# Kernel tuning notes

Hardware: AMD Instinct MI355X
Metric: run time of the kernel (lower is better)

## Reference

```python
import jax, jax.numpy as jnp
import numpy as np

EPS_L2 = 1e-12  # torch F.normalize eps
EPS_NORM = 1e-5  # ZeroCenteredRMSNorm eps


def _linear(x, W, b):
    return x @ W.T + b


def _silu(x):
    return x * jax.nn.sigmoid(x)


def _l2norm(x):
    n = jnp.sqrt(jnp.sum(x * x, axis=-1, keepdims=True))
    return x / jnp.maximum(n, EPS_L2)


def _dwconv_causal(x, w, b):
    # x: [B,S,d]; w: [d,1,4] (torch depthwise conv weight); causal pad 3 left
    y = jax.lax.conv_general_dilated(
        x.transpose(0, 2, 1), w, window_strides=(1,), padding=[(3, 0)],
        dimension_numbers=('NCH', 'OIH', 'NCH'), feature_group_count=w.shape[0])
    return y.transpose(0, 2, 1) + b


def _zc_rmsnorm(x, weight):
    xm = x - jnp.mean(x, axis=-1, keepdims=True)
    var = jnp.mean(xm * xm, axis=-1, keepdims=True)
    return xm * jax.lax.rsqrt(var + EPS_NORM) * weight


def _gated_delta_core(q, k, v, alpha, beta):
    # q,k,v: [B,S,d]; alpha,beta: [B,S]
    B, S, d = q.shape
    S0 = jnp.zeros((B, d, d), dtype=q.dtype)

    def step(St, inp):
        qt, kt, vt, at, bt = inp  # [B,d],[B,d],[B,d],[B],[B]
        # S @ (a*(I - b k k^T)) = a*(S - b*(S k) k^T)   (rank-1 update, same math)
        Sk = jnp.einsum('bij,bj->bi', St, kt)            # [B,d]
        a = at[:, None, None]
        b = bt[:, None, None]
        Sn = a * (St - b * Sk[:, :, None] * kt[:, None, :]) + b * vt[:, :, None] * kt[:, None, :]
        ot = jnp.einsum('bij,bj->bi', Sn, qt)            # [B,d]
        return Sn, ot

    xs = (q.transpose(1, 0, 2), k.transpose(1, 0, 2), v.transpose(1, 0, 2),
          alpha.T, beta.T)
    _, outs = jax.lax.scan(step, S0, xs)  # outs: [S,B,d]
    return outs.transpose(1, 0, 2)


def setup_inputs() -> dict:
    key = jax.random.key(0)
    ks = jax.random.split(key, 16)
    B, S, d = 8, 2048, 512
    w = lambda k, shape: (jax.random.normal(k, shape, jnp.float32) * 0.02)
    return {
        'x': jax.random.normal(ks[0], (B, S, d), jnp.float32),
        'Wq': w(ks[1], (d, d)), 'bq': jnp.zeros((d,), jnp.float32),
        'Wk': w(ks[2], (d, d)), 'bk': jnp.zeros((d,), jnp.float32),
        'Wv': w(ks[3], (d, d)), 'bv': jnp.zeros((d,), jnp.float32),
        'Wa': w(ks[4], (1, d)), 'ba': jnp.zeros((1,), jnp.float32),
        'Wb': w(ks[5], (1, d)), 'bb': jnp.zeros((1,), jnp.float32),
        'cwq': w(ks[6], (d, 1, 4)), 'cbq': jnp.zeros((d,), jnp.float32),
        'cwk': w(ks[7], (d, 1, 4)), 'cbk': jnp.zeros((d,), jnp.float32),
        'cwv': w(ks[8], (d, 1, 4)), 'cbv': jnp.zeros((d,), jnp.float32),
        'norm_w': jnp.ones((d,), jnp.float32),
        'Wg': w(ks[9], (d, d)), 'bg': jnp.zeros((d,), jnp.float32),
        'Wo': w(ks[10], (d, d)), 'bo': jnp.zeros((d,), jnp.float32),
    }


def reference(x, Wq, bq, Wk, bk, Wv, bv, Wa, ba, Wb, bb,
              cwq, cbq, cwk, cbk, cwv, cbv, norm_w, Wg, bg, Wo, bo):
    q_c = _dwconv_causal(_linear(x, Wq, bq), cwq, cbq)
    k_c = _dwconv_causal(_linear(x, Wk, bk), cwk, cbk)
    v_c = _dwconv_causal(_linear(x, Wv, bv), cwv, cbv)
    q = _l2norm(_silu(q_c))
    k = _l2norm(_silu(k_c))
    v = _silu(v_c)
    alpha = jax.nn.sigmoid(_linear(x, Wa, ba))[..., 0]  # [B,S]
    beta = jax.nn.sigmoid(_linear(x, Wb, bb))[..., 0]   # [B,S]
    gdn = _gated_delta_core(q, k, v, alpha, beta)       # [B,S,d]
    gdn = _zc_rmsnorm(gdn, norm_w)
    gate = _silu(_linear(x, Wg, bg))
    return _linear(gdn * gate, Wo, bo)
```

## Files before the change

### kernel.cpp

```cpp
#include <hip/hip_runtime.h>
#include <math.h>

typedef unsigned short u16;
typedef unsigned int u32;
typedef short short8 __attribute__((ext_vector_type(8)));
typedef float f32x4 __attribute__((ext_vector_type(4)));

#define B_ 8
#define S_ 2048
#define D_ 512
#define N_ (B_ * S_)
#define ND_ ((size_t)N_ * D_)
#define CC_ 32
#define NC_ (S_ / CC_)
#define SV_ 16

__device__ __forceinline__ u16 f2bf(float f) {
  union { float f; u32 i; } v; v.f = f;
  u32 i = v.i;
  i += 0x7FFFu + ((i >> 16) & 1u);
  return (u16)(i >> 16);
}
__device__ __forceinline__ float bf2f(u16 u) {
  union { u32 i; float f; } v; v.i = ((u32)u) << 16; return v.f;
}
__device__ __forceinline__ float sigm(float x) { return 1.0f / (1.0f + expf(-x)); }

__global__ __launch_bounds__(256) void cvt_bf16(const float* __restrict__ s,
                                                u16* __restrict__ d, int n)
{
  const int i = (blockIdx.x * 256 + threadIdx.x) * 4;
  if (i < n) {
    const float4 v = *(const float4*)(s + i);
    ushort4 o;
    o.x = f2bf(v.x); o.y = f2bf(v.y); o.z = f2bf(v.z); o.w = f2bf(v.w);
    *(ushort4*)(d + i) = o;
  }
}

__global__ __launch_bounds__(256) void cvt_w5(
    const float* __restrict__ w0, const float* __restrict__ w1,
    const float* __restrict__ w2, const float* __restrict__ w3,
    const float* __restrict__ w4, u16* __restrict__ d)
{
  const int z = blockIdx.y;
  const float* s = (z == 0) ? w0 : (z == 1) ? w1 : (z == 2) ? w2 : (z == 3) ? w3 : w4;
  u16* o = d + (size_t)z * 512 * 512;
  const int i = (blockIdx.x * 256 + threadIdx.x) * 4;
  const float4 v = *(const float4*)(s + i);
  ushort4 t;
  t.x = f2bf(v.x); t.y = f2bf(v.y); t.z = f2bf(v.z); t.w = f2bf(v.w);
  *(ushort4*)(o + i) = t;
}

__global__ __launch_bounds__(256) void gemm_bt(
    const u16* __restrict__ A, const u16* __restrict__ W,
    const float* __restrict__ bias, float* __restrict__ out)
{
  __shared__ u16 As[128 * 40];
  __shared__ u16 Bs[128 * 40];
  const int tid = threadIdx.x;
  const int lane = tid & 63, wave = tid >> 6;
  const int wm = (wave >> 1) * 64, wn = (wave & 1) * 64;
  const int l15 = lane & 15, quad = lane >> 4;
  const int m0 = blockIdx.x * 128, n0 = blockIdx.y * 128;
  const int r0 = tid >> 2;
  const int kc0 = (tid & 3) * 8;

  f32x4 acc[4][4];
#pragma unroll
  for (int i = 0; i < 4; i++)
#pragma unroll
    for (int j = 0; j < 4; j++) acc[i][j] = (f32x4){0.f, 0.f, 0.f, 0.f};

  for (int k0 = 0; k0 < 512; k0 += 32) {
    uint4 a0 = *(const uint4*)(A + (size_t)(m0 + r0) * 512 + k0 + kc0);
    uint4 a1 = *(const uint4*)(A + (size_t)(m0 + r0 + 64) * 512 + k0 + kc0);
    uint4 b0 = *(const uint4*)(W + (size_t)(n0 + r0) * 512 + k0 + kc0);
    uint4 b1 = *(const uint4*)(W + (size_t)(n0 + r0 + 64) * 512 + k0 + kc0);
    __syncthreads();
    *(uint4*)(As + r0 * 40 + kc0) = a0;
    *(uint4*)(As + (r0 + 64) * 40 + kc0) = a1;
    *(uint4*)(Bs + r0 * 40 + kc0) = b0;
    *(uint4*)(Bs + (r0 + 64) * 40 + kc0) = b1;
    __syncthreads();
    short8 af[4], bf[4];
#pragma unroll
    for (int mt = 0; mt < 4; mt++) af[mt] = *(const short8*)(As + (wm + mt * 16 + l15) * 40 + quad * 8);
#pragma unroll
    for (int nt = 0; nt < 4; nt++) bf[nt] = *(const short8*)(Bs + (wn + nt * 16 + l15) * 40 + quad * 8);
#pragma unroll
    for (int mt = 0; mt < 4; mt++)
#pragma unroll
      for (int nt = 0; nt < 4; nt++)
        acc[mt][nt] = __builtin_amdgcn_mfma_f32_16x16x32_bf16(af[mt], bf[nt], acc[mt][nt], 0, 0, 0);
  }
#pragma unroll
  for (int mt = 0; mt < 4; mt++) {
#pragma unroll
    for (int nt = 0; nt < 4; nt++) {
      const int col = n0 + wn + nt * 16 + l15;
      const float bcol = bias[col];
#pragma unroll
      for (int r = 0; r < 4; r++) {
        const int row = m0 + wm + mt * 16 + quad * 4 + r;
        out[(size_t)row * 512 + col] = acc[mt][nt][r] + bcol;
      }
    }
  }
}

__global__ __launch_bounds__(256) void ab_kernel(
    const float* __restrict__ x, const float* __restrict__ Wa, const float* __restrict__ ba,
    const float* __restrict__ Wb, const float* __restrict__ bb,
    float* __restrict__ alpha, float* __restrict__ beta)
{
  const int lane = threadIdx.x & 63, wave = threadIdx.x >> 6;
  const int row = blockIdx.x * 4 + wave;
  const float4 x0 = *(const float4*)(x + (size_t)row * 512 + lane * 8);
  const float4 x1 = *(const float4*)(x + (size_t)row * 512 + lane * 8 + 4);
  const float4 a0 = *(const float4*)(Wa + lane * 8);
  const float4 a1 = *(const float4*)(Wa + lane * 8 + 4);
  const float4 b0 = *(const float4*)(Wb + lane * 8);
  const float4 b1 = *(const float4*)(Wb + lane * 8 + 4);
  float da = x0.x*a0.x + x0.y*a0.y + x0.z*a0.z + x0.w*a0.w
           + x1.x*a1.x + x1.y*a1.y + x1.z*a1.z + x1.w*a1.w;
  float db = x0.x*b0.x + x0.y*b0.y + x0.z*b0.z + x0.w*b0.w
           + x1.x*b1.x + x1.y*b1.y + x1.z*b1.z + x1.w*b1.w;
#pragma unroll
  for (int m = 32; m >= 1; m >>= 1) { da += __shfl_xor(da, m, 64); db += __shfl_xor(db, m, 64); }
  if (lane == 0) {
    alpha[row] = sigm(da + ba[0]);
    beta[row]  = sigm(db + bb[0]);
  }
}

__global__ __launch_bounds__(256) void conv_act(
    const float* __restrict__ lq, const float* __restrict__ lk, const float* __restrict__ lv,
    const float* __restrict__ cwq, const float* __restrict__ cbq,
    const float* __restrict__ cwk, const float* __restrict__ cbk,
    const float* __restrict__ cwv, const float* __restrict__ cbv,
    u16* __restrict__ oq, u16* __restrict__ ok, float* __restrict__ ov)
{
  __shared__ float red[4];
  const int row = blockIdx.x;
  const int z = blockIdx.y;
  const int b = row / S_, t = row - b * S_;
  const float* lin = (z == 0) ? lq : (z == 1) ? lk : lv;
  const float* cw = (z == 0) ? cwq : (z == 1) ? cwk : cwv;
  const float* cb = (z == 0) ? cbq : (z == 1) ? cbk : cbv;
  const int tid = threadIdx.x;
  float s[2]; float ssq = 0.f;
#pragma unroll
  for (int e = 0; e < 2; e++) {
    const int ch = tid + e * 256;
    float acc = cb[ch];
#pragma unroll
    for (int tau = 0; tau < 4; tau++) {
      const int tt = t - 3 + tau;
      if (tt >= 0) acc = fmaf(lin[(size_t)(b * S_ + tt) * D_ + ch], cw[ch * 4 + tau], acc);
    }
    const float sv = acc * sigm(acc);
    s[e] = sv; ssq = fmaf(sv, sv, ssq);
  }
  if (z < 2) {
    float v = ssq;
#pragma unroll
    for (int m = 32; m >= 1; m >>= 1) v += __shfl_xor(v, m, 64);
    if ((tid & 63) == 0) red[tid >> 6] = v;
    __syncthreads();
    const float tot = red[0] + red[1] + red[2] + red[3];
    const float scale = 1.0f / fmaxf(sqrtf(tot), 1e-12f);
    u16* outp = (z == 0) ? oq : ok;
    outp[(size_t)row * D_ + tid] = f2bf(s[0] * scale);
    outp[(size_t)row * D_ + tid + 256] = f2bf(s[1] * scale);
  } else {
    ov[(size_t)row * D_ + tid] = s[0];
    ov[(size_t)row * D_ + tid + 256] = s[1];
  }
}

__global__ __launch_bounds__(256) void transpose_k(
    const u16* __restrict__ kh, u16* __restrict__ khT)
{
  __shared__ u16 T[64][68];
  const int b = blockIdx.z;
  const int t0 = blockIdx.x * 64;
  const int c0 = blockIdx.y * 64;
  const int tid = threadIdx.x;
  const int tr = tid >> 4;
  const int c4 = (tid & 15) * 4;
#pragma unroll
  for (int i = 0; i < 4; i++) {
    const int t = tr + i * 16;
    ushort4 v = *(const ushort4*)(kh + ((size_t)(b * S_ + t0 + t)) * 512 + c0 + c4);
    T[c4 + 0][t] = v.x; T[c4 + 1][t] = v.y; T[c4 + 2][t] = v.z; T[c4 + 3][t] = v.w;
  }
  __syncthreads();
#pragma unroll
  for (int i = 0; i < 4; i++) {
    const int ch = tr + i * 16;
    ushort4 v = *(const ushort4*)&T[ch][c4];
    *(ushort4*)(khT + ((size_t)(b * 512 + c0 + ch)) * S_ + t0 + c4) = v;
  }
}

__global__ __launch_bounds__(256) void prepass(
    const u16* __restrict__ kh, const u16* __restrict__ qh,
    float* __restrict__ vbU,
    const float* __restrict__ alpha, const float* __restrict__ beta,
    u16* __restrict__ Ag, float* __restrict__ gg, u16* __restrict__ Wc)
{
  __shared__ float KK[32][33];
  __shared__ float QK[32][33];
  __shared__ float Ml[32][33];
  __shared__ float Xs[32][33];
  __shared__ u16 Xb[32 * 40];
  __shared__ u16 VT[512 * 40];
  __shared__ float lg[32], cum[32], bet[32], gams[32];
  const int bc = blockIdx.x;
  const int b = bc >> 6, c = bc & 63;
  const int t0 = c * CC_;
  const int tid = threadIdx.x, lane = tid & 63, w = tid >> 6;
  const int l15 = lane & 15, quad = lane >> 4;
  const size_t rb = (size_t)b * S_ + t0;

  if (tid < 32) { lg[tid] = logf(alpha[b * S_ + t0 + tid]); bet[tid] = beta[b * S_ + t0 + tid]; }
  __syncthreads();
  if (tid < 32) {
    float s = 0.f;
    for (int u = 0; u <= tid; u++) s += lg[u];
    cum[tid] = s;
    gams[tid] = expf(s);
  }
  const int mi = w >> 1, ni = w & 1;
  f32x4 ck = (f32x4){0.f,0.f,0.f,0.f}, cq = ck;
#pragma unroll
  for (int kt = 0; kt < 16; kt++) {
    const int kc = kt * 32 + quad * 8;
    short8 afk = *(const short8*)(kh + (rb + mi * 16 + l15) * 512 + kc);
    short8 afq = *(const short8*)(qh + (rb + mi * 16 + l15) * 512 + kc);
    short8 bk  = *(const short8*)(kh + (rb + ni * 16 + l15) * 512 + kc);
    ck = __builtin_amdgcn_mfma_f32_16x16x32_bf16(afk, bk, ck, 0, 0, 0);
    cq = __builtin_amdgcn_mfma_f32_16x16x32_bf16(afq, bk, cq, 0, 0, 0);
  }
#pragma unroll
  for (int r = 0; r < 4; r++) {
    KK[mi * 16 + quad * 4 + r][ni * 16 + l15] = ck[r];
    QK[mi * 16 + quad * 4 + r][ni * 16 + l15] = cq[r];
  }
  __syncthreads();
  if (tid < 32) {
    gg[(size_t)bc * 64 + tid] = gams[tid];
    gg[(size_t)bc * 64 + 32 + tid] = expf(cum[31] - cum[tid]);
  }
#pragma unroll
  for (int rep = 0; rep < 4; rep++) {
    const int e = tid + rep * 256;
    const int t = e >> 5, s = e & 31;
    const float er = expf(cum[t] - cum[s]);
    Ml[t][s] = (s < t) ? bet[t] * er * KK[t][s] : 0.f;
    Ag[(size_t)bc * 1024 + t * 32 + s] = (s <= t) ? f2bf(QK[t][s] * er) : (u16)0;
  }
#pragma unroll
  for (int rep = 0; rep < 8; rep++) {
    const int e = tid + rep * 256;
    const int v = e & 511, so = e >> 9;
    short8 pk;
#pragma unroll
    for (int j = 0; j < 8; j++) {
      const int s = so * 8 + j;
      pk[j] = (short)f2bf(bet[s] * vbU[(rb + s) * 512 + v]);
    }
    *(short8*)&VT[v * 40 + so * 8] = pk;
  }
  __syncthreads();
  if (w == 0 && lane < 32) {
    const int j = lane;
    Xs[0][j] = (j == 0) ? 1.f : 0.f;
    for (int t = 1; t < 32; t++) {
      float a = (t == j) ? 1.f : 0.f;
      for (int u = 0; u < t; u++) a = fmaf(-Ml[t][u], Xs[u][j], a);
      Xs[t][j] = a;
    }
  }
  __syncthreads();
#pragma unroll
  for (int rep = 0; rep < 4; rep++) {
    const int e = tid + rep * 256;
    const int t = e >> 5, s = e & 31;
    Xb[t * 40 + s] = f2bf(Xs[t][s]);
  }
  __syncthreads();
  short8 xa[2];
  xa[0] = *(const short8*)&Xb[l15 * 40 + quad * 8];
  xa[1] = *(const short8*)&Xb[(16 + l15) * 40 + quad * 8];
#pragma unroll
  for (int ntr = 0; ntr < 8; ntr++) {
    const int nt = w * 8 + ntr;
    short8 bv = *(const short8*)&VT[(nt * 16 + l15) * 40 + quad * 8];
#pragma unroll
    for (int mt = 0; mt < 2; mt++) {
      f32x4 g = (f32x4){0.f, 0.f, 0.f, 0.f};
      g = __builtin_amdgcn_mfma_f32_16x16x32_bf16(xa[mt], bv, g, 0, 0, 0);
#pragma unroll
      for (int r = 0; r < 4; r++)
        vbU[(rb + mt * 16 + quad * 4 + r) * 512 + nt * 16 + l15] = g[r];
    }
  }
  __syncthreads();
#pragma unroll
  for (int rep = 0; rep < 8; rep++) {
    const int e = tid + rep * 256;
    const int v = e & 511, so = e >> 9;
    short8 pk;
#pragma unroll
    for (int j = 0; j < 8; j++) {
      const int s = so * 8 + j;
      pk[j] = (short)f2bf(bet[s] * gams[s] * bf2f(kh[(rb + s) * 512 + v]));
    }
    *(short8*)&VT[v * 40 + so * 8] = pk;
  }
  __syncthreads();
#pragma unroll
  for (int ntr = 0; ntr < 8; ntr++) {
    const int nt = w * 8 + ntr;
    short8 bv = *(const short8*)&VT[(nt * 16 + l15) * 40 + quad * 8];
#pragma unroll
    for (int mt = 0; mt < 2; mt++) {
      f32x4 g = (f32x4){0.f, 0.f, 0.f, 0.f};
      g = __builtin_amdgcn_mfma_f32_16x16x32_bf16(xa[mt], bv, g, 0, 0, 0);
#pragma unroll
      for (int r = 0; r < 4; r++)
        Wc[(size_t)bc * 16384 + (mt * 16 + quad * 4 + r) * 512 + nt * 16 + l15] = f2bf(g[r]);
    }
  }
}

__global__ __launch_bounds__(512) void scan_chunk(
    const u16* __restrict__ qh, const u16* __restrict__ khT,
    const u16* __restrict__ Wc, const float* __restrict__ U,
    const u16* __restrict__ Ag, const float* __restrict__ gg,
    float* __restrict__ gdn)
{
  __shared__ u16 S_A[16 * 520];
  __shared__ float P[2][2][32][16];
  __shared__ u16 Ct_T[16 * 40];
  __shared__ u16 Cr_T[16 * 40];
  __shared__ float OB[32][17];
  __shared__ float gam[32], grc[32];
  const int b = blockIdx.y;
  const int iv0 = blockIdx.x * SV_;
  const int tid = threadIdx.x, lane = tid & 63, w = tid >> 6;
  const int l15 = lane & 15, quad = lane >> 4;
  const int ttile = w & 1, mat = (w >> 1) & 1, khalf = w >> 2;
  const size_t bS = (size_t)b * S_;
  const int ct = tid >> 4, cv = tid & 15;

  f32x4 acc[4];
#pragma unroll
  for (int mt = 0; mt < 4; mt++) acc[mt] = (f32x4){0.f, 0.f, 0.f, 0.f};

  short8 nbf[8], ntk[4], nagf = {};
  float nUv = 0.f, ngam = 0.f, ngrc = 0.f;

#define SCAN_LOAD(CN) do {                                                          \
    const int t0n_ = (CN) * CC_;                                                    \
    const int bcn_ = b * 64 + (CN);                                                 \
    const u16* bsrc_ = mat ? (qh + (bS + t0n_ + ttile * 16 + l15) * 512 + khalf * 256) \
                           : (Wc + ((size_t)bcn_ * 32 + ttile * 16 + l15) * 512 + khalf * 256); \
    _Pragma("unroll")                                                               \
    for (int kt_ = 0; kt_ < 8; kt_++)                                               \
      nbf[kt_] = *(const short8*)(bsrc_ + kt_ * 32 + quad * 8);                     \
    _Pragma("unroll")                                                               \
    for (int mt_ = 0; mt_ < 4; mt_++)                                               \
      ntk[mt_] = *(const short8*)(khT + ((size_t)(b * 512 + w * 64 + mt_ * 16 + l15)) * S_ + t0n_ + quad * 8); \
    nUv = U[(bS + t0n_ + ct) * 512 + iv0 + cv];                                     \
    if (w < 2) nagf = *(const short8*)(Ag + (size_t)bcn_ * 1024 + (w * 16 + l15) * 32 + quad * 8); \
    if (tid < 32) { ngam = gg[(size_t)bcn_ * 64 + tid]; ngrc = gg[(size_t)bcn_ * 64 + 32 + tid]; } \
  } while (0)

  SCAN_LOAD(0);

#pragma unroll 1
  for (int c = 0; c < NC_; c++) {
    const int t0 = c * CC_;
    short8 bfrag[8], tk[4], agf;
#pragma unroll
    for (int kt = 0; kt < 8; kt++) bfrag[kt] = nbf[kt];
#pragma unroll
    for (int mt = 0; mt < 4; mt++) tk[mt] = ntk[mt];
    agf = nagf;
    const float Uv = nUv, gamv = ngam, grcv = ngrc;
    const int cn = (c + 1 < NC_) ? c + 1 : c;
    SCAN_LOAD(cn);
    if (tid < 32) { gam[tid] = gamv; grc[tid] = grcv; }
#pragma unroll
    for (int mt = 0; mt < 4; mt++) {
      ushort4 p;
      p.x = f2bf(acc[mt][0]); p.y = f2bf(acc[mt][1]);
      p.z = f2bf(acc[mt][2]); p.w = f2bf(acc[mt][3]);
      *(ushort4*)&S_A[l15 * 520 + w * 64 + mt * 16 + quad * 4] = p;
    }
    __syncthreads();
    f32x4 g = (f32x4){0.f, 0.f, 0.f, 0.f};
#pragma unroll
    for (int kt = 0; kt < 8; kt++) {
      short8 af = *(const short8*)&S_A[l15 * 520 + khalf * 256 + kt * 32 + quad * 8];
      g = __builtin_amdgcn_mfma_f32_16x16x32_bf16(af, bfrag[kt], g, 0, 0, 0);
    }
    *(f32x4*)&P[mat][khalf][ttile * 16 + l15][quad * 4] = g;
    __syncthreads();
    const float gCs = gam[31];
    {
      const float T1 = P[0][0][ct][cv] + P[0][1][ct][cv];
      const float T2 = P[1][0][ct][cv] + P[1][1][ct][cv];
      const float ctv = Uv - T1;
      Ct_T[cv * 40 + ct] = f2bf(ctv);
      Cr_T[cv * 40 + ct] = f2bf(ctv * grc[ct]);
      OB[ct][cv] = gam[ct] * T2;
    }
    __syncthreads();
    short8 bcf = *(const short8*)&Cr_T[l15 * 40 + quad * 8];
#pragma unroll
    for (int mt = 0; mt < 4; mt++) {
      acc[mt] = acc[mt] * gCs;
      acc[mt] = __builtin_amdgcn_mfma_f32_16x16x32_bf16(tk[mt], bcf, acc[mt], 0, 0, 0);
    }
    if (w < 2) {
      short8 ctf = *(const short8*)&Ct_T[l15 * 40 + quad * 8];
      f32x4 oo;
#pragma unroll
      for (int r = 0; r < 4; r++) oo[r] = OB[w * 16 + quad * 4 + r][l15];
      oo = __builtin_amdgcn_mfma_f32_16x16x32_bf16(agf, ctf, oo, 0, 0, 0);
#pragma unroll
      for (int r = 0; r < 4; r++)
        gdn[(bS + t0 + w * 16 + quad * 4 + r) * 512 + iv0 + l15] = oo[r];
    }
  }
#undef SCAN_LOAD
}

__global__ __launch_bounds__(256) void norm_gate(
    const float* __restrict__ gdn, const float* __restrict__ lg,
    const float* __restrict__ nw, u16* __restrict__ h)
{
  __shared__ float red[8];
  const int row = blockIdx.x, tid = threadIdx.x;
  const size_t base = (size_t)row * D_;
  const float g0 = gdn[base + tid], g1 = gdn[base + tid + 256];
  float sm = g0 + g1;
#pragma unroll
  for (int m = 32; m >= 1; m >>= 1) sm += __shfl_xor(sm, m, 64);
  if ((tid & 63) == 0) red[tid >> 6] = sm;
  __syncthreads();
  const float mean = (red[0] + red[1] + red[2] + red[3]) * (1.0f / 512.0f);
  const float x0 = g0 - mean, x1 = g1 - mean;
  float sq = x0 * x0 + x1 * x1;
#pragma unroll
  for (int m = 32; m >= 1; m >>= 1) sq += __shfl_xor(sq, m, 64);
  if ((tid & 63) == 0) red[4 + (tid >> 6)] = sq;
  __syncthreads();
  const float var = (red[4] + red[5] + red[6] + red[7]) * (1.0f / 512.0f);
  const float rst = rsqrtf(var + 1e-5f);
  const float gl0 = lg[base + tid];
  h[base + tid] = f2bf(x0 * rst * nw[tid] * (gl0 * sigm(gl0)));
  const float gl1 = lg[base + tid + 256];
  h[base + tid + 256] = f2bf(x1 * rst * nw[tid + 256] * (gl1 * sigm(gl1)));
}

extern "C" void kernel_launch(void* const* d_in, const int* in_sizes, int n_in,
                              void* d_out, int out_size, void* d_ws, size_t ws_size,
                              hipStream_t stream)
{
  const float* x   = (const float*)d_in[0];
  const float* Wq  = (const float*)d_in[1];
  const float* bq  = (const float*)d_in[2];
  const float* Wk  = (const float*)d_in[3];
  const float* bk  = (const float*)d_in[4];
  const float* Wv  = (const float*)d_in[5];
  const float* bv  = (const float*)d_in[6];
  const float* Wa  = (const float*)d_in[7];
  const float* ba  = (const float*)d_in[8];
  const float* Wb  = (const float*)d_in[9];
  const float* bb  = (const float*)d_in[10];
  const float* cwq = (const float*)d_in[11];
  const float* cbq = (const float*)d_in[12];
  const float* cwk = (const float*)d_in[13];
  const float* cbk = (const float*)d_in[14];
  const float* cwv = (const float*)d_in[15];
  const float* cbv = (const float*)d_in[16];
  const float* nw  = (const float*)d_in[17];
  const float* Wg  = (const float*)d_in[18];
  const float* bg  = (const float*)d_in[19];
  const float* Wo  = (const float*)d_in[20];
  const float* bo  = (const float*)d_in[21];

  float* ws    = (float*)d_ws;
  float* lin_q = ws;
  float* lin_k = ws + ND_;
  float* lin_v = ws + 2 * ND_;
  float* lin_g = ws + 3 * ND_;
  float* vb    = ws + 4 * ND_;
  u16*   qh    = (u16*)(ws + 5 * ND_);
  u16*   kh    = qh + ND_;
  float* alpha = ws + 6 * ND_;
  float* beta  = alpha + N_;
  u16*   xb    = (u16*)(beta + N_);
  u16*   wq_b  = xb + ND_;
  u16*   wk_b  = wq_b + 512 * 512;
  u16*   wv_b  = wk_b + 512 * 512;
  u16*   wg_b  = wv_b + 512 * 512;
  u16*   wo_b  = wg_b + 512 * 512;

  u16*   khT   = (u16*)lin_k;
  u16*   Agb   = khT + ND_;
  float* ggb   = (float*)(Agb + (size_t)512 * 1024);
  u16*   Wcb   = (u16*)lin_v;
  float* gdn   = lin_q;
  u16*   h     = (u16*)lin_v;

  const int NW = 512 * 512;
  cvt_bf16<<<(int)(ND_ / 1024), 256, 0, stream>>>(x, xb, (int)ND_);
  cvt_w5<<<dim3(NW / 1024, 5), 256, 0, stream>>>(Wq, Wk, Wv, Wg, Wo, wq_b);

  dim3 gg4(128, 4);
  gemm_bt<<<gg4, 256, 0, stream>>>(xb, wq_b, bq, lin_q);
  gemm_bt<<<gg4, 256, 0, stream>>>(xb, wk_b, bk, lin_k);
  gemm_bt<<<gg4, 256, 0, stream>>>(xb, wv_b, bv, lin_v);
  gemm_bt<<<gg4, 256, 0, stream>>>(xb, wg_b, bg, lin_g);
  ab_kernel<<<N_ / 4, 256, 0, stream>>>(x, Wa, ba, Wb, bb, alpha, beta);
  conv_act<<<dim3(N_, 3), 256, 0, stream>>>(lin_q, lin_k, lin_v,
                                            cwq, cbq, cwk, cbk, cwv, cbv, qh, kh, vb);
  transpose_k<<<dim3(S_ / 64, D_ / 64, B_), 256, 0, stream>>>(kh, khT);
  prepass<<<B_ * NC_, 256, 0, stream>>>(kh, qh, vb, alpha, beta, Agb, ggb, Wcb);
  scan_chunk<<<dim3(D_ / SV_, B_), 512, 0, stream>>>(qh, khT, Wcb, vb, Agb, ggb, gdn);
  norm_gate<<<N_, 256, 0, stream>>>(gdn, lin_g, nw, h);
  gemm_bt<<<gg4, 256, 0, stream>>>(h, wo_b, bo, (float*)d_out);
}
```

Measured before the change: 581.6 us.

## Use LDS-only barriers in chunked scan and pad shared-memory strides

Each __syncthreads in the scan loop becomes a custom barrier that waits only on LDS counters. The next chunk's global prefetches can then stay in flight across the barriers instead of being drained. Per-chunk gamma factors are now loaded straight into registers by every thread rather than broadcast through shared memory. Shared-array row strides change from 520/40 to 530/42 to reduce bank conflicts. The risk is that the new strides break 16-byte alignment for the vector LDS reads and writes, which could split accesses or misbehave.

```diff
diff --git a/kernel.cpp b/kernel.cpp
--- a/kernel.cpp
+++ b/kernel.cpp
@@ -14,6 +14,8 @@
 #define CC_ 32
 #define NC_ (S_ / CC_)
 #define SV_ 16
+#define SAS 530
+#define CTS 42
 
 __device__ __forceinline__ u16 f2bf(float f) {
   union { float f; u32 i; } v; v.f = f;
@@ -25,6 +27,12 @@
   union { u32 i; float f; } v; v.i = ((u32)u) << 16; return v.f;
 }
 __device__ __forceinline__ float sigm(float x) { return 1.0f / (1.0f + expf(-x)); }
+
+__device__ __forceinline__ void bar_lds() {
+  asm volatile("s_waitcnt lgkmcnt(0)" ::: "memory");
+  __builtin_amdgcn_s_barrier();
+  asm volatile("" ::: "memory");
+}
 
 __global__ __launch_bounds__(256) void cvt_bf16(const float* __restrict__ s,
                                                 u16* __restrict__ d, int n)
@@ -343,12 +351,11 @@
     const u16* __restrict__ Ag, const float* __restrict__ gg,
     float* __restrict__ gdn)
 {
-  __shared__ u16 S_A[16 * 520];
+  __shared__ u16 S_A[16 * SAS];
   __shared__ float P[2][2][32][16];
-  __shared__ u16 Ct_T[16 * 40];
-  __shared__ u16 Cr_T[16 * 40];
+  __shared__ u16 Ct_T[16 * CTS];
+  __shared__ u16 Cr_T[16 * CTS];
   __shared__ float OB[32][17];
-  __shared__ float gam[32], grc[32];
   const int b = blockIdx.y;
   const int iv0 = blockIdx.x * SV_;
   const int tid = threadIdx.x, lane = tid & 63, w = tid >> 6;
@@ -362,7 +369,7 @@
   for (int mt = 0; mt < 4; mt++) acc[mt] = (f32x4){0.f, 0.f, 0.f, 0.f};
 
   short8 nbf[8], ntk[4], nagf = {};
-  float nUv = 0.f, ngam = 0.f, ngrc = 0.f;
+  float nUv = 0.f, ngam = 0.f, ngrc = 0.f, ngCs = 0.f;
 
 #define SCAN_LOAD(CN) do {                                                          \
     const int t0n_ = (CN) * CC_;                                                    \
@@ -377,7 +384,9 @@
       ntk[mt_] = *(const short8*)(khT + ((size_t)(b * 512 + w * 64 + mt_ * 16 + l15)) * S_ + t0n_ + quad * 8); \
     nUv = U[(bS + t0n_ + ct) * 512 + iv0 + cv];                                     \
     if (w < 2) nagf = *(const short8*)(Ag + (size_t)bcn_ * 1024 + (w * 16 + l15) * 32 + quad * 8); \
-    if (tid < 32) { ngam = gg[(size_t)bcn_ * 64 + tid]; ngrc = gg[(size_t)bcn_ * 64 + 32 + tid]; } \
+    ngam = gg[(size_t)bcn_ * 64 + ct];                                              \
+    ngrc = gg[(size_t)bcn_ * 64 + 32 + ct];                                         \
+    ngCs = gg[(size_t)bcn_ * 64 + 31];                                              \
   } while (0)
 
   SCAN_LOAD(0);
@@ -391,44 +400,42 @@
 #pragma unroll
     for (int mt = 0; mt < 4; mt++) tk[mt] = ntk[mt];
     agf = nagf;
-    const float Uv = nUv, gamv = ngam, grcv = ngrc;
+    const float Uv = nUv, gamv = ngam, grcv = ngrc, gCsv = ngCs;
     const int cn = (c + 1 < NC_) ? c + 1 : c;
     SCAN_LOAD(cn);
-    if (tid < 32) { gam[tid] = gamv; grc[tid] = grcv; }
 #pragma unroll
     for (int mt = 0; mt < 4; mt++) {
       ushort4 p;
       p.x = f2bf(acc[mt][0]); p.y = f2bf(acc[mt][1]);
       p.z = f2bf(acc[mt][2]); p.w = f2bf(acc[mt][3]);
-      *(ushort4*)&S_A[l15 * 520 + w * 64 + mt * 16 + quad * 4] = p;
-    }
-    __syncthreads();
+      *(ushort4*)&S_A[l15 * SAS + w * 64 + mt * 16 + quad * 4] = p;
+    }
+    bar_lds();
     f32x4 g = (f32x4){0.f, 0.f, 0.f, 0.f};
 #pragma unroll
     for (int kt = 0; kt < 8; kt++) {
-      short8 af = *(const short8*)&S_A[l15 * 520 + khalf * 256 + kt * 32 + quad * 8];
+      short8 af = *(const short8*)&S_A[l15 * SAS + khalf * 256 + kt * 32 + quad * 8];
       g = __builtin_amdgcn_mfma_f32_16x16x32_bf16(af, bfrag[kt], g, 0, 0, 0);
     }
     *(f32x4*)&P[mat][khalf][ttile * 16 + l15][quad * 4] = g;
-    __syncthreads();
-    const float gCs = gam[31];
+    bar_lds();
     {
       const float T1 = P[0][0][ct][cv] + P[0][1][ct][cv];
       const float T2 = P[1][0][ct][cv] + P[1][1][ct][cv];
       const float ctv = Uv - T1;
-      Ct_T[cv * 40 + ct] = f2bf(ctv);
-      Cr_T[cv * 40 + ct] = f2bf(ctv * grc[ct]);
-      OB[ct][cv] = gam[ct] * T2;
-    }
-    __syncthreads();
-    short8 bcf = *(const short8*)&Cr_T[l15 * 40 + quad * 8];
+      Ct_T[cv * CTS + ct] = f2bf(ctv);
+      Cr_T[cv * CTS + ct] = f2bf(ctv * grcv);
+      OB[ct][cv] = gamv * T2;
+    }
+    bar_lds();
+    short8 bcf = *(const short8*)&Cr_T[l15 * CTS + quad * 8];
 #pragma unroll
     for (int mt = 0; mt < 4; mt++) {
-      acc[mt] = acc[mt] * gCs;
+      acc[mt] = acc[mt] * gCsv;
       acc[mt] = __builtin_amdgcn_mfma_f32_16x16x32_bf16(tk[mt], bcf, acc[mt], 0, 0, 0);
     }
     if (w < 2) {
-      short8 ctf = *(const short8*)&Ct_T[l15 * 40 + quad * 8];
+      short8 ctf = *(const short8*)&Ct_T[l15 * CTS + quad * 8];
       f32x4 oo;
 #pragma unroll
       for (int r = 0; r < 4; r++) oo[r] = OB[w * 16 + quad * 4 + r][l15];
```

New measurement: 600.5 us. +3.3%, slower.
